# Performance work log

Measured on AMD Instinct MI355X. Metric: run time of the kernel, lower is better.

The kernel has to match this reference:

```python
import jax, jax.numpy as jnp
import numpy as np

GROUP_SIZE = 64
BITS = 4
VALS_PER_WORD = 32 // BITS  # 8 nibbles per uint32


def setup_inputs() -> dict:
    key = jax.random.key(0)
    ks = jax.random.split(key, 7)
    B, S, I, O = 4, 2048, 4096, 4096
    G = I // GROUP_SIZE
    x = jax.random.normal(ks[0], (B, S, I), dtype=jnp.float32)
    channel_scale = jax.random.uniform(ks[1], (1, 1, I), dtype=jnp.float32, minval=0.5, maxval=1.5)
    # packed int4 weights: random uint32 words
    qweight = jax.random.randint(ks[2], (O, I // VALS_PER_WORD), 0, 2147483647, dtype=jnp.int32).astype(jnp.uint32)
    q_perm = jax.random.permutation(ks[3], I).astype(jnp.int32)
    scales = jax.random.uniform(ks[4], (O, G), dtype=jnp.float32, minval=0.001, maxval=0.02)
    zeros = jax.random.normal(ks[5], (O, G), dtype=jnp.float32) * 0.05
    bias = jax.random.normal(ks[6], (O,), dtype=jnp.float32) * 0.02
    return {"x": x, "channel_scale": channel_scale, "qweight": qweight,
            "q_perm": q_perm, "scales": scales, "zeros": zeros, "bias": bias}


def _dequantize(qweight, scales, zeros):
    # qweight: (O, I/8) uint32 -> nibbles little-endian within each word
    O, packed = qweight.shape
    shifts = (jnp.arange(VALS_PER_WORD, dtype=jnp.uint32) * BITS)  # (8,)
    wq = (qweight[:, :, None] >> shifts[None, None, :]) & jnp.uint32((1 << BITS) - 1)
    wq = wq.reshape(O, packed * VALS_PER_WORD).astype(jnp.float32)  # (O, I)
    # mlx dequantize: w = wq * scale + bias(zeros), per group of GROUP_SIZE along input dim
    s = jnp.repeat(scales, GROUP_SIZE, axis=1)  # (O, I)
    z = jnp.repeat(zeros, GROUP_SIZE, axis=1)   # (O, I)
    return wq * s + z


def reference(x, channel_scale, qweight, q_perm, scales, zeros, bias):
    # per-channel scale
    x = x * channel_scale
    # optional permute gather along feature axis
    x = jnp.take(x, q_perm, axis=-1)
    # group-wise int4 dequant matmul (transpose=True: out = x @ W^T)
    W = _dequantize(qweight, scales, zeros)  # (O, I)
    out = jnp.einsum('bsi,oi->bso', x, W)
    return out + bias
```

## Files before the change

### kernel.cpp

```cpp
#include <hip/hip_runtime.h>

typedef unsigned int u32;
typedef unsigned char u8;

#define M_DIM 8192
#define K_DIM 4096
#define N_DIM 4096
#define GROUPS 64

typedef int intx4 __attribute__((ext_vector_type(4)));

__device__ __forceinline__ void gload_lds16(const void* g, void* l) {
  __builtin_amdgcn_global_load_lds(
      (const __attribute__((address_space(1))) void*)g,
      (__attribute__((address_space(3))) void*)l, 16, 0, 0);
}

__device__ __forceinline__ float block_absmax(float amax, float* red) {
#pragma unroll
  for (int off = 32; off; off >>= 1)
    amax = fmaxf(amax, __shfl_xor(amax, off, 64));
  const int wave = threadIdx.x >> 6;
  if ((threadIdx.x & 63) == 0) red[wave] = amax;
  __syncthreads();
  return fmaxf(fmaxf(red[0], red[1]), fmaxf(red[2], red[3]));
}

__device__ __forceinline__ u32 pack4(const float* v, float inv) {
  u32 r = 0;
#pragma unroll
  for (int i = 0; i < 4; ++i) {
    int q = (int)__builtin_rintf(v[i] * inv);
    q = q > 127 ? 127 : (q < -127 ? -127 : q);
    r |= ((u32)(u8)(char)q) << (8 * i);
  }
  return r;
}

__global__ __launch_bounds__(256) void prep_all(
    const float* __restrict__ x, const float* __restrict__ cs,
    const u32* __restrict__ qw, const int* __restrict__ perm,
    const float* __restrict__ scales, const float* __restrict__ zeros,
    u8* __restrict__ xq, u8* __restrict__ wq,
    float* __restrict__ sx, float* __restrict__ sw) {
  __shared__ float rowbuf[K_DIM];
  __shared__ float red[4];
  const int t = threadIdx.x;
  const int base = t * 16;
  if (blockIdx.x < N_DIM) {
    const int o = blockIdx.x;
    const u32* qrow = qw + (size_t)o * (K_DIM / 8);
    const float s = scales[o * GROUPS + (t >> 2)];
    const float z = zeros[o * GROUPS + (t >> 2)];
    uint2 w = *(const uint2*)(qrow + 2 * t);
    int4 p0 = *(const int4*)(perm + base + 0);
    int4 p1 = *(const int4*)(perm + base + 4);
    int4 p2 = *(const int4*)(perm + base + 8);
    int4 p3 = *(const int4*)(perm + base + 12);
    float v[16];
    float amax = 0.f;
#pragma unroll
    for (int n = 0; n < 8; ++n) {
      v[n]     = (float)((w.x >> (4 * n)) & 15u) * s + z;
      v[8 + n] = (float)((w.y >> (4 * n)) & 15u) * s + z;
      amax = fmaxf(amax, fmaxf(fabsf(v[n]), fabsf(v[8 + n])));
    }
    rowbuf[p0.x] = v[0];  rowbuf[p0.y] = v[1];
    rowbuf[p0.z] = v[2];  rowbuf[p0.w] = v[3];
    rowbuf[p1.x] = v[4];  rowbuf[p1.y] = v[5];
    rowbuf[p1.z] = v[6];  rowbuf[p1.w] = v[7];
    rowbuf[p2.x] = v[8];  rowbuf[p2.y] = v[9];
    rowbuf[p2.z] = v[10]; rowbuf[p2.w] = v[11];
    rowbuf[p3.x] = v[12]; rowbuf[p3.y] = v[13];
    rowbuf[p3.z] = v[14]; rowbuf[p3.w] = v[15];
    amax = block_absmax(amax, red);
    amax = fmaxf(amax, 1e-20f);
    const float inv = 127.0f / amax;
    uint4 p;
    p.x = pack4(rowbuf + base + 0, inv);
    p.y = pack4(rowbuf + base + 4, inv);
    p.z = pack4(rowbuf + base + 8, inv);
    p.w = pack4(rowbuf + base + 12, inv);
    *(uint4*)(wq + (size_t)o * K_DIM + base) = p;
    if (t == 0) sw[o] = amax * (1.0f / 127.0f);
  } else {
    const size_t m = blockIdx.x - N_DIM;
    const float* xr = x + m * K_DIM;
    float v[16];
    float amax = 0.f;
#pragma unroll
    for (int j = 0; j < 4; ++j) {
      float4 xv = *(const float4*)(xr + base + j * 4);
      float4 cv = *(const float4*)(cs + base + j * 4);
      v[j * 4 + 0] = xv.x * cv.x;
      v[j * 4 + 1] = xv.y * cv.y;
      v[j * 4 + 2] = xv.z * cv.z;
      v[j * 4 + 3] = xv.w * cv.w;
#pragma unroll
      for (int i = 0; i < 4; ++i) amax = fmaxf(amax, fabsf(v[j * 4 + i]));
    }
    amax = block_absmax(amax, red);
    amax = fmaxf(amax, 1e-20f);
    const float inv = 127.0f / amax;
    uint4 p;
    p.x = pack4(v + 0, inv);
    p.y = pack4(v + 4, inv);
    p.z = pack4(v + 8, inv);
    p.w = pack4(v + 12, inv);
    *(uint4*)(xq + m * K_DIM + base) = p;
    if (t == 0) sx[m] = amax * (1.0f / 127.0f);
  }
}

#define BM 128
#define BN 128
#define BK 64
#define KTILES (K_DIM / BK)

__global__ __launch_bounds__(256, 2) void gemm_i8(
    const u8* __restrict__ A, const u8* __restrict__ B,
    const float* __restrict__ sx, const float* __restrict__ sw,
    const float* __restrict__ bias, float* __restrict__ out) {
  __shared__ __align__(16) u8 As[2][BM * BK];
  __shared__ __align__(16) u8 Bs[2][BN * BK];
  const int tid = threadIdx.x;
  const int lane = tid & 63;
  const int wave = tid >> 6;
  const int wm = wave >> 1;
  const int wn = wave & 1;
  const int q = lane >> 4, lr = lane & 15;
  const int qs = q ^ ((lr >> 1) & 3);

  const int wg = blockIdx.x;
  const int swzwg = (wg & 7) * 256 + (wg >> 3);
  const int blockN = (swzwg & 31) * BN;
  const int blockM = (swzwg >> 5) * BM;

  const char* Abase = (const char*)(A + (size_t)blockM * K_DIM);
  const char* Bbase = (const char*)(B + (size_t)blockN * K_DIM);

  const int c0 = tid, c1 = tid + 256;
  const int kc0 = (c0 & 3) ^ ((c0 >> 3) & 3);
  const int kc1 = (c1 & 3) ^ ((c1 >> 3) & 3);
  const size_t gOff0 = (size_t)(c0 >> 2) * K_DIM + kc0 * 16;
  const size_t gOff1 = (size_t)(c1 >> 2) * K_DIM + kc1 * 16;
  const int dOff0 = c0 * 16, dOff1 = c1 * 16;

  const int aoff = (wm * 64 + lr) * 64 + qs * 16;
  const int boff = (wn * 64 + lr) * 64 + qs * 16;

  intx4 acc[4][4];
#pragma unroll
  for (int i = 0; i < 4; ++i)
#pragma unroll
    for (int j = 0; j < 4; ++j) acc[i][j] = (intx4)0;

  auto stage = [&](int t, int b) {
    const size_t koff = (size_t)t * BK;
    gload_lds16(Abase + gOff0 + koff, &As[b][dOff0]);
    gload_lds16(Abase + gOff1 + koff, &As[b][dOff1]);
    gload_lds16(Bbase + gOff0 + koff, &Bs[b][dOff0]);
    gload_lds16(Bbase + gOff1 + koff, &Bs[b][dOff1]);
  };

  stage(0, 0);
  asm volatile("s_waitcnt vmcnt(0)" ::: "memory");
  asm volatile("s_barrier" ::: "memory");

  for (int t = 0; t < KTILES; ++t) {
    const int cur = t & 1;
    if (t + 1 < KTILES) stage(t + 1, cur ^ 1);

    const u8* Ab = &As[cur][0];
    const u8* Bb = &Bs[cur][0];
    intx4 af[4], bf[4];
#pragma unroll
    for (int mi = 0; mi < 4; ++mi)
      af[mi] = *(const intx4*)(Ab + aoff + mi * 1024);
#pragma unroll
    for (int ni = 0; ni < 4; ++ni)
      bf[ni] = *(const intx4*)(Bb + boff + ni * 1024);

    __builtin_amdgcn_s_setprio(1);
#pragma unroll
    for (int mi = 0; mi < 4; ++mi)
#pragma unroll
      for (int ni = 0; ni < 4; ++ni)
        acc[mi][ni] = __builtin_amdgcn_mfma_i32_16x16x64_i8(
            af[mi], bf[ni], acc[mi][ni], 0, 0, 0);
    __builtin_amdgcn_s_setprio(0);

    if (t + 1 < KTILES) {
      asm volatile("s_waitcnt vmcnt(0)" ::: "memory");
      asm volatile("s_barrier" ::: "memory");
    }
  }

#pragma unroll
  for (int ni = 0; ni < 4; ++ni) {
    const int col = blockN + wn * 64 + ni * 16 + lr;
    const float swv = sw[col];
    const float bv = bias[col];
#pragma unroll
    for (int mi = 0; mi < 4; ++mi) {
      const int row0 = blockM + wm * 64 + mi * 16 + q * 4;
#pragma unroll
      for (int r = 0; r < 4; ++r) {
        const float s = sx[row0 + r] * swv;
        out[(size_t)(row0 + r) * N_DIM + col] = (float)acc[mi][ni][r] * s + bv;
      }
    }
  }
}

extern "C" void kernel_launch(void* const* d_in, const int* in_sizes, int n_in,
                              void* d_out, int out_size, void* d_ws, size_t ws_size,
                              hipStream_t stream) {
  const float* x      = (const float*)d_in[0];
  const float* cs     = (const float*)d_in[1];
  const u32*   qw     = (const u32*)d_in[2];
  const int*   perm   = (const int*)d_in[3];
  const float* scales = (const float*)d_in[4];
  const float* zeros  = (const float*)d_in[5];
  const float* bias   = (const float*)d_in[6];
  float* out = (float*)d_out;

  u8* xq = (u8*)d_ws;
  u8* wq = xq + (size_t)M_DIM * K_DIM;
  float* sx = (float*)(wq + (size_t)N_DIM * K_DIM);
  float* sw = sx + M_DIM;

  hipLaunchKernelGGL(prep_all, dim3(N_DIM + M_DIM), dim3(256), 0, stream,
                     x, cs, qw, perm, scales, zeros, xq, wq, sx, sw);
  hipLaunchKernelGGL(gemm_i8, dim3((M_DIM / BM) * (N_DIM / BN)), dim3(256), 0,
                     stream, xq, wq, sx, sw, bias, out);
}
```

Measured before the change: 400.7 us.

## Triple-buffer GEMM LDS staging and quantize activations one row per wave

The int8 GEMM moves from double to triple buffering of the A/B tiles in LDS, prefetching two k-tiles ahead and waiting with vmcnt(4) so one tile's loads stay in flight during compute. The activation quantization path now gives each wave a full row, using only a wave shuffle reduction and no block barrier, and launches a quarter as many blocks. Triple buffering raises LDS use to 48KB per block, which may reduce occupancy below the two blocks per CU the launch bounds target. The per-wave row path holds 64 floats per thread, raising register pressure in the prep kernel.

```diff
diff --git a/kernel.cpp b/kernel.cpp
--- a/kernel.cpp
+++ b/kernel.cpp
@@ -14,16 +14,6 @@
   __builtin_amdgcn_global_load_lds(
       (const __attribute__((address_space(1))) void*)g,
       (__attribute__((address_space(3))) void*)l, 16, 0, 0);
-}
-
-__device__ __forceinline__ float block_absmax(float amax, float* red) {
-#pragma unroll
-  for (int off = 32; off; off >>= 1)
-    amax = fmaxf(amax, __shfl_xor(amax, off, 64));
-  const int wave = threadIdx.x >> 6;
-  if ((threadIdx.x & 63) == 0) red[wave] = amax;
-  __syncthreads();
-  return fmaxf(fmaxf(red[0], red[1]), fmaxf(red[2], red[3]));
 }
 
 __device__ __forceinline__ u32 pack4(const float* v, float inv) {
@@ -46,8 +36,8 @@
   __shared__ float rowbuf[K_DIM];
   __shared__ float red[4];
   const int t = threadIdx.x;
-  const int base = t * 16;
   if (blockIdx.x < N_DIM) {
+    const int base = t * 16;
     const int o = blockIdx.x;
     const u32* qrow = qw + (size_t)o * (K_DIM / 8);
     const float s = scales[o * GROUPS + (t >> 2)];
@@ -73,7 +63,12 @@
     rowbuf[p2.z] = v[10]; rowbuf[p2.w] = v[11];
     rowbuf[p3.x] = v[12]; rowbuf[p3.y] = v[13];
     rowbuf[p3.z] = v[14]; rowbuf[p3.w] = v[15];
-    amax = block_absmax(amax, red);
+#pragma unroll
+    for (int off = 32; off; off >>= 1)
+      amax = fmaxf(amax, __shfl_xor(amax, off, 64));
+    if ((t & 63) == 0) red[t >> 6] = amax;
+    __syncthreads();
+    amax = fmaxf(fmaxf(red[0], red[1]), fmaxf(red[2], red[3]));
     amax = fmaxf(amax, 1e-20f);
     const float inv = 127.0f / amax;
     uint4 p;
@@ -84,31 +79,42 @@
     *(uint4*)(wq + (size_t)o * K_DIM + base) = p;
     if (t == 0) sw[o] = amax * (1.0f / 127.0f);
   } else {
-    const size_t m = blockIdx.x - N_DIM;
+    const int wave = t >> 6, lane = t & 63;
+    const size_t m = (size_t)(blockIdx.x - N_DIM) * 4 + wave;
     const float* xr = x + m * K_DIM;
-    float v[16];
+    float v[64];
     float amax = 0.f;
 #pragma unroll
     for (int j = 0; j < 4; ++j) {
-      float4 xv = *(const float4*)(xr + base + j * 4);
-      float4 cv = *(const float4*)(cs + base + j * 4);
-      v[j * 4 + 0] = xv.x * cv.x;
-      v[j * 4 + 1] = xv.y * cv.y;
-      v[j * 4 + 2] = xv.z * cv.z;
-      v[j * 4 + 3] = xv.w * cv.w;
-#pragma unroll
-      for (int i = 0; i < 4; ++i) amax = fmaxf(amax, fabsf(v[j * 4 + i]));
-    }
-    amax = block_absmax(amax, red);
+      const int col = j * 1024 + lane * 16;
+#pragma unroll
+      for (int u = 0; u < 4; ++u) {
+        float4 xv = *(const float4*)(xr + col + u * 4);
+        float4 cv = *(const float4*)(cs + col + u * 4);
+        float* vp = v + j * 16 + u * 4;
+        vp[0] = xv.x * cv.x;
+        vp[1] = xv.y * cv.y;
+        vp[2] = xv.z * cv.z;
+        vp[3] = xv.w * cv.w;
+        amax = fmaxf(amax, fmaxf(fmaxf(fabsf(vp[0]), fabsf(vp[1])),
+                                 fmaxf(fabsf(vp[2]), fabsf(vp[3]))));
+      }
+    }
+#pragma unroll
+    for (int off = 32; off; off >>= 1)
+      amax = fmaxf(amax, __shfl_xor(amax, off, 64));
     amax = fmaxf(amax, 1e-20f);
     const float inv = 127.0f / amax;
-    uint4 p;
-    p.x = pack4(v + 0, inv);
-    p.y = pack4(v + 4, inv);
-    p.z = pack4(v + 8, inv);
-    p.w = pack4(v + 12, inv);
-    *(uint4*)(xq + m * K_DIM + base) = p;
-    if (t == 0) sx[m] = amax * (1.0f / 127.0f);
+#pragma unroll
+    for (int j = 0; j < 4; ++j) {
+      uint4 p;
+      p.x = pack4(v + j * 16 + 0, inv);
+      p.y = pack4(v + j * 16 + 4, inv);
+      p.z = pack4(v + j * 16 + 8, inv);
+      p.w = pack4(v + j * 16 + 12, inv);
+      *(uint4*)(xq + m * K_DIM + j * 1024 + lane * 16) = p;
+    }
+    if (lane == 0) sx[m] = amax * (1.0f / 127.0f);
   }
 }
 
@@ -121,8 +127,8 @@
     const u8* __restrict__ A, const u8* __restrict__ B,
     const float* __restrict__ sx, const float* __restrict__ sw,
     const float* __restrict__ bias, float* __restrict__ out) {
-  __shared__ __align__(16) u8 As[2][BM * BK];
-  __shared__ __align__(16) u8 Bs[2][BN * BK];
+  __shared__ __align__(16) u8 As[3][BM * BK];
+  __shared__ __align__(16) u8 Bs[3][BN * BK];
   const int tid = threadIdx.x;
   const int lane = tid & 63;
   const int wave = tid >> 6;
@@ -164,15 +170,16 @@
   };
 
   stage(0, 0);
-  asm volatile("s_waitcnt vmcnt(0)" ::: "memory");
+  stage(1, 1);
+  asm volatile("s_waitcnt vmcnt(4)" ::: "memory");
   asm volatile("s_barrier" ::: "memory");
 
+  int bc = 0, bs = 2;
   for (int t = 0; t < KTILES; ++t) {
-    const int cur = t & 1;
-    if (t + 1 < KTILES) stage(t + 1, cur ^ 1);
-
-    const u8* Ab = &As[cur][0];
-    const u8* Bb = &Bs[cur][0];
+    if (t + 2 < KTILES) stage(t + 2, bs);
+
+    const u8* Ab = &As[bc][0];
+    const u8* Bb = &Bs[bc][0];
     intx4 af[4], bf[4];
 #pragma unroll
     for (int mi = 0; mi < 4; ++mi)
@@ -190,10 +197,15 @@
             af[mi], bf[ni], acc[mi][ni], 0, 0, 0);
     __builtin_amdgcn_s_setprio(0);
 
-    if (t + 1 < KTILES) {
+    if (t + 2 < KTILES) {
+      asm volatile("s_waitcnt vmcnt(4)" ::: "memory");
+    } else if (t + 1 < KTILES) {
       asm volatile("s_waitcnt vmcnt(0)" ::: "memory");
-      asm volatile("s_barrier" ::: "memory");
-    }
+    }
+    if (t + 1 < KTILES) asm volatile("s_barrier" ::: "memory");
+
+    bc = (bc == 2) ? 0 : bc + 1;
+    bs = (bs == 2) ? 0 : bs + 1;
   }
 
 #pragma unroll
@@ -230,7 +242,7 @@
   float* sx = (float*)(wq + (size_t)N_DIM * K_DIM);
   float* sw = sx + M_DIM;
 
-  hipLaunchKernelGGL(prep_all, dim3(N_DIM + M_DIM), dim3(256), 0, stream,
+  hipLaunchKernelGGL(prep_all, dim3(N_DIM + M_DIM / 4), dim3(256), 0, stream,
                      x, cs, qw, perm, scales, zeros, xq, wq, sx, sw);
   hipLaunchKernelGGL(gemm_i8, dim3((M_DIM / BM) * (N_DIM / BN)), dim3(256), 0,
                      stream, xq, wq, sx, sw, bias, out);
```

Result: no change. 404.9 us (+1.1%).
